# Performance work log

Hardware: AMD Instinct MI355X
Metric: run time of the kernel (lower is better)

The kernel has to match this reference:

```python
import jax, jax.numpy as jnp
import numpy as np
import math

D = 768
H = 8
DH = D // H
T = 4
MODES = 16
NUM_CLASSES = 14


def setup_inputs() -> dict:
    key = jax.random.key(0)
    ks = iter(jax.random.split(key, 64))
    B, S = 256, 512
    inp = {}
    inp['x_feat'] = jax.random.normal(next(ks), (B, S, D), dtype=jnp.float32)
    # attention pool
    inp['pool_w'] = jax.random.normal(next(ks), (D, 1), dtype=jnp.float32) * 0.02
    inp['pool_b'] = jnp.zeros((1,), dtype=jnp.float32)
    # per-block params, stacked over T
    def pstack(shape, scale=0.02):
        return jax.random.normal(next(ks), (T,) + shape, dtype=jnp.float32) * scale
    inp['w_q'] = pstack((D, D)); inp['w_k'] = pstack((D, D)); inp['w_v'] = pstack((D, D))
    inp['b_qkv'] = jnp.zeros((T, 3 * D), dtype=jnp.float32)
    inp['w_o'] = pstack((D, D)); inp['b_o'] = jnp.zeros((T, D), dtype=jnp.float32)
    inp['ln1_g'] = jnp.ones((T, D), dtype=jnp.float32); inp['ln1_b'] = jnp.zeros((T, D), dtype=jnp.float32)
    inp['ln2_g'] = jnp.ones((T, D), dtype=jnp.float32); inp['ln2_b'] = jnp.zeros((T, D), dtype=jnp.float32)
    inp['scale_real'] = pstack((MODES, D)); inp['scale_imag'] = pstack((MODES, D))
    inp['proj_w'] = pstack((D, D)); inp['proj_b'] = jnp.zeros((T, D), dtype=jnp.float32)
    inp['bn_g'] = jnp.ones((T, D), dtype=jnp.float32); inp['bn_b'] = jnp.zeros((T, D), dtype=jnp.float32)
    inp['gate'] = jnp.full((T,), 0.5, dtype=jnp.float32)
    inp['scale_attn'] = jnp.ones((T,), dtype=jnp.float32)
    inp['scale_denoise'] = jnp.ones((T,), dtype=jnp.float32)
    # fuse MLP + classifier
    inp['f1_w'] = jax.random.normal(next(ks), (D, 256), dtype=jnp.float32) * 0.02
    inp['f1_b'] = jnp.zeros((256,), dtype=jnp.float32)
    inp['f1_bn_g'] = jnp.ones((256,), dtype=jnp.float32); inp['f1_bn_b'] = jnp.zeros((256,), dtype=jnp.float32)
    inp['f2_w'] = jax.random.normal(next(ks), (256, 128), dtype=jnp.float32) * 0.02
    inp['f2_b'] = jnp.zeros((128,), dtype=jnp.float32)
    inp['f2_bn_g'] = jnp.ones((128,), dtype=jnp.float32); inp['f2_bn_b'] = jnp.zeros((128,), dtype=jnp.float32)
    inp['cls_w'] = jax.random.normal(next(ks), (128, NUM_CLASSES), dtype=jnp.float32) * 0.02
    inp['cls_b'] = jnp.zeros((NUM_CLASSES,), dtype=jnp.float32)
    return inp


def _layernorm(x, g, b, eps=1e-5):
    mu = jnp.mean(x, axis=-1, keepdims=True)
    var = jnp.var(x, axis=-1, keepdims=True)
    return (x - mu) * jax.lax.rsqrt(var + eps) * g + b


def _bn_eval(x, g, b, eps=1e-5):
    # eval-mode BatchNorm1d with running_mean=0, running_var=1
    return x * (g / jnp.sqrt(1.0 + eps)) + b


def _forward(x_feat, pool_w, pool_b, w_q, w_k, w_v, b_qkv, w_o, b_o,
             ln1_g, ln1_b, ln2_g, ln2_b, scale_real, scale_imag, proj_w, proj_b,
             bn_g, bn_b, gate, scale_attn, scale_denoise,
             f1_w, f1_b, f1_bn_g, f1_bn_b, f2_w, f2_b, f2_bn_g, f2_bn_b,
             cls_w, cls_b):
    B, S, _ = x_feat.shape
    # attention pool: softmax over seq of a scalar score per token
    scores = x_feat @ pool_w + pool_b          # [B,S,1]
    weights = jax.nn.softmax(scores, axis=1)
    z = jnp.sum(weights * x_feat, axis=1)      # [B,D]

    def classify(z):
        h = jax.nn.relu(_bn_eval(z @ f1_w + f1_b, f1_bn_g, f1_bn_b))
        h = jax.nn.relu(_bn_eval(h @ f2_w + f2_b, f2_bn_g, f2_bn_b))
        return h @ cls_w + cls_b

    logits_sum = jnp.zeros((B, NUM_CLASSES), dtype=x_feat.dtype)
    for t in range(T):
        bq, bk, bv = b_qkv[t, :D], b_qkv[t, D:2 * D], b_qkv[t, 2 * D:]
        # query: single token z [B,1,D]; keys/values: x_feat [B,S,D]
        q = (z @ w_q[t].T + bq).reshape(B, H, 1, DH)
        k = (x_feat @ w_k[t].T + bk).reshape(B, S, H, DH).transpose(0, 2, 1, 3)
        v = (x_feat @ w_v[t].T + bv).reshape(B, S, H, DH).transpose(0, 2, 1, 3)
        att = jax.nn.softmax(jnp.einsum('bhqd,bhsd->bhqs', q, k) / math.sqrt(DH), axis=-1)
        o = jnp.einsum('bhqs,bhsd->bhqd', att, v).reshape(B, D)
        z_attn = o @ w_o[t].T + b_o[t]
        z1 = _layernorm(z + scale_attn[t] * z_attn, ln1_g[t], ln1_b[t])
        # fft denoise: keep first MODES freq bins scaled by mean of complex filter per mode
        z_freq = jnp.fft.fft(z1, axis=1)                        # [B,D] complex
        filt = jnp.mean(scale_real[t] + 1j * scale_imag[t], axis=1)  # [MODES] complex
        keep = z_freq[:, :MODES] * filt[None, :]
        z_filtered = jnp.concatenate([keep, jnp.zeros((B, D - MODES), dtype=z_freq.dtype)], axis=1)
        z_spatial = jnp.fft.ifft(z_filtered, axis=1).real
        z_den = z_spatial @ proj_w[t].T + proj_b[t]
        z2 = _layernorm(z1 + scale_denoise[t] * z_den, ln2_g[t], ln2_b[t])
        g = jax.nn.sigmoid(gate[t])
        z3 = g * z2 + (1.0 - g) * z
        z = _bn_eval(z3, bn_g[t], bn_b[t])
        logits_sum = logits_sum + classify(z)
    return logits_sum / T


def reference(x_feat, pool_w, pool_b, w_q, w_k, w_v, b_qkv, w_o, b_o,
              ln1_g, ln1_b, ln2_g, ln2_b, scale_real, scale_imag, proj_w, proj_b,
              bn_g, bn_b, gate, scale_attn, scale_denoise,
              f1_w, f1_b, f1_bn_g, f1_bn_b, f2_w, f2_b, f2_bn_g, f2_bn_b,
              cls_w, cls_b):
    return _forward(x_feat, pool_w, pool_b, w_q, w_k, w_v, b_qkv, w_o, b_o,
                    ln1_g, ln1_b, ln2_g, ln2_b, scale_real, scale_imag, proj_w, proj_b,
                    bn_g, bn_b, gate, scale_attn, scale_denoise,
                    f1_w, f1_b, f1_bn_g, f1_bn_b, f2_w, f2_b, f2_bn_g, f2_bn_b,
                    cls_w, cls_b)
```

## Files before the change

### kernel.cpp

```cpp
#include <hip/hip_runtime.h>
#include <math.h>


#define DEV __device__ __forceinline__

typedef unsigned int   uint32;
typedef unsigned short ushort_t;
typedef __attribute__((ext_vector_type(8))) short bf16x8;
typedef __attribute__((ext_vector_type(4))) float f32x4;
typedef __attribute__((ext_vector_type(2))) float f32x2;

constexpr int Bv  = 256;
constexpr int Sv  = 512;
constexpr int Dv  = 768;
constexpr int Hv  = 8;
constexpr int DHv = 96;
constexpr int NCv = 14;

constexpr size_t ZL  = 196608;
constexpr size_t XWL = 1572864;
constexpr size_t WL  = 2359296;
constexpr size_t WT  = 589824;

DEV float4 ld4(const float* p) { return *reinterpret_cast<const float4*>(p); }

DEV ushort_t f2bf(float f) {
    uint32 u = __float_as_uint(f);
    u += 0x7FFFu + ((u >> 16) & 1u);
    return (ushort_t)(u >> 16);
}
DEV float bf2f(ushort_t h) { return __uint_as_float((uint32)h << 16); }
DEV void split2(float f, ushort_t& hi, ushort_t& lo) {
    hi = f2bf(f);
    lo = f2bf(f - bf2f(hi));
}
DEV uint2 pack4(float4 v) {
    return make_uint2((uint32)f2bf(v.x) | ((uint32)f2bf(v.y) << 16),
                      (uint32)f2bf(v.z) | ((uint32)f2bf(v.w) << 16));
}
DEV float bflo(uint32 u) { return __uint_as_float(u << 16); }
DEV float bfhi(uint32 u) { return __uint_as_float(u & 0xFFFF0000u); }

DEV f32x2 bfpair(uint32 u) {
    f32x2 r;
    r.x = __uint_as_float(u << 16);
    r.y = __uint_as_float(u & 0xFFFF0000u);
    return r;
}

DEV f32x2 pkfma(f32x2 a, f32x2 b, f32x2 c) {
    f32x2 d;
    asm("v_pk_fma_f32 %0, %1, %2, %3" : "=v"(d) : "v"(a), "v"(b), "v"(c));
    return d;
}

DEV void glds16(const void* g, void* l) {
    __builtin_amdgcn_global_load_lds(
        (const __attribute__((address_space(1))) void*)g,
        (__attribute__((address_space(3))) void*)l, 16, 0, 0);
}

__global__ __launch_bounds__(512, 4)
void pool_cvt_kernel(const float* __restrict__ x, const float* __restrict__ pool_w,
                     ushort_t* __restrict__ xbf,
                     float* __restrict__ pacc, float2* __restrict__ pml)
{
    __shared__ float qks[Dv];
    const int b = blockIdx.x, half = blockIdx.y;
    const int tid = threadIdx.x, wave = tid >> 6, lane = tid & 63;
    for (int i = tid; i < Dv / 4; i += 512)
        *reinterpret_cast<float4*>(&qks[i * 4]) = ld4(pool_w + i * 4);
    __syncthreads();

    const int row0 = half * 256 + wave * 32;
    const float* base = x + ((size_t)b * Sv + row0) * Dv + 4 * lane;

    float4 acc[3];
#pragma unroll
    for (int j = 0; j < 3; ++j) acc[j] = make_float4(0.f, 0.f, 0.f, 0.f);
    float m = -INFINITY, l = 0.f;

    float4 c0[3], c1[3];
#pragma unroll
    for (int j = 0; j < 3; ++j) { c0[j] = ld4(base + 256 * j); c1[j] = ld4(base + Dv + 256 * j); }

    for (int it = 0; it < 16; ++it) {
        float4 n0_[3], n1_[3];
        if (it < 15) {
            const float* nb = base + (size_t)(2 * it + 2) * Dv;
#pragma unroll
            for (int j = 0; j < 3; ++j) { n0_[j] = ld4(nb + 256 * j); n1_[j] = ld4(nb + Dv + 256 * j); }
        }
        ushort_t* ob = xbf + ((size_t)b * Sv + row0 + 2 * it) * Dv + 4 * lane;
#pragma unroll
        for (int j = 0; j < 3; ++j) *reinterpret_cast<uint2*>(ob + 256 * j) = pack4(c0[j]);
#pragma unroll
        for (int j = 0; j < 3; ++j) *reinterpret_cast<uint2*>(ob + Dv + 256 * j) = pack4(c1[j]);
        float p0 = 0.f, p1 = 0.f;
#pragma unroll
        for (int j = 0; j < 3; ++j) {
            const float4 q4 = *reinterpret_cast<const float4*>(&qks[4 * lane + 256 * j]);
            p0 = fmaf(q4.x, c0[j].x, p0); p0 = fmaf(q4.y, c0[j].y, p0);
            p0 = fmaf(q4.z, c0[j].z, p0); p0 = fmaf(q4.w, c0[j].w, p0);
            p1 = fmaf(q4.x, c1[j].x, p1); p1 = fmaf(q4.y, c1[j].y, p1);
            p1 = fmaf(q4.z, c1[j].z, p1); p1 = fmaf(q4.w, c1[j].w, p1);
        }
#pragma unroll
        for (int dd = 1; dd < 64; dd <<= 1) { p0 += __shfl_xor(p0, dd); p1 += __shfl_xor(p1, dd); }
        float mx = fmaxf(p0, p1);
        if (mx > m) {
            float r = __expf(m - mx); l *= r;
#pragma unroll
            for (int j = 0; j < 3; ++j) { acc[j].x *= r; acc[j].y *= r; acc[j].z *= r; acc[j].w *= r; }
            m = mx;
        }
        float w0 = __expf(p0 - m), w1 = __expf(p1 - m);
        l += w0 + w1;
#pragma unroll
        for (int j = 0; j < 3; ++j) {
            acc[j].x = fmaf(w1, c1[j].x, fmaf(w0, c0[j].x, acc[j].x));
            acc[j].y = fmaf(w1, c1[j].y, fmaf(w0, c0[j].y, acc[j].y));
            acc[j].z = fmaf(w1, c1[j].z, fmaf(w0, c0[j].z, acc[j].z));
            acc[j].w = fmaf(w1, c1[j].w, fmaf(w0, c0[j].w, acc[j].w));
        }
        if (it < 15) {
#pragma unroll
            for (int j = 0; j < 3; ++j) { c0[j] = n0_[j]; c1[j] = n1_[j]; }
        }
    }
    const int p = half * 8 + wave;
    const size_t pidx = (size_t)p * 256 + b;
#pragma unroll
    for (int j = 0; j < 3; ++j)
        *reinterpret_cast<float4*>(&pacc[pidx * Dv + 4 * lane + 256 * j]) = acc[j];
    if (lane == 0) pml[pidx] = make_float2(m, l);
}

__global__ __launch_bounds__(512, 4)
void attn_flash_kernel(const ushort_t* __restrict__ xbf, const float* __restrict__ Qk,
                       float* __restrict__ pacc, float2* __restrict__ pml, float scale)
{
    __shared__ ushort_t xs[2][16 * Dv];
    const int b = blockIdx.x, half = blockIdx.y;
    const int tid = threadIdx.x, wave = tid >> 6, lane = tid & 63;
    const int s0base = half * 256;

    const float* qp = Qk + ((size_t)b * Hv + wave) * Dv;
    f32x2 q2[6];
    {
        float4 a = ld4(qp + 8 * lane);
        float4 c = ld4(qp + 8 * lane + 4);
        float4 e = ld4(qp + 512 + 4 * lane);
        q2[0] = (f32x2){a.x, a.y}; q2[1] = (f32x2){a.z, a.w};
        q2[2] = (f32x2){c.x, c.y}; q2[3] = (f32x2){c.z, c.w};
        q2[4] = (f32x2){e.x, e.y}; q2[5] = (f32x2){e.z, e.w};
    }
    f32x2 acc2[6];
#pragma unroll
    for (int c = 0; c < 6; ++c) acc2[c] = (f32x2){0.f, 0.f};
    float m = -INFINITY, l = 0.f;

    auto stage = [&](int i, int buf) {
#pragma unroll
        for (int r = 0; r < 3; ++r) {
            int idx = wave * 3 + r;
            int off = idx * 1024 + lane * 16;
            int q   = off >> 9;
            int row = (q * 683) >> 11;
            int seg = q - row * 3;
            int colb = (seg << 9) + (off & 511);
            const char* src = (const char*)xbf +
                ((size_t)((size_t)b * Sv + s0base + i * 16 + row) * Dv) * 2 + colb;
            glds16(src, (char*)xs[buf] + idx * 1024);
        }
    };

    stage(0, 0);
    int cur = 0;
    for (int i = 0; i < 16; ++i) {
        __builtin_amdgcn_s_barrier();
        if (i < 15) {
            stage(i + 1, cur ^ 1);
            asm volatile("s_waitcnt vmcnt(3)" ::: "memory");
        } else {
            asm volatile("s_waitcnt vmcnt(0)" ::: "memory");
        }
        __builtin_amdgcn_s_barrier();
        __builtin_amdgcn_sched_barrier(0);

        const ushort_t* xt = xs[cur];
#pragma unroll
        for (int ch = 0; ch < 4; ++ch) {
            f32x2 xr[4][6];
            float s4[4];
#pragma unroll
            for (int j = 0; j < 4; ++j) {
                const ushort_t* rp = xt + (ch * 4 + j) * Dv;
                uint4 u0 = *reinterpret_cast<const uint4*>(rp + 8 * lane);
                uint2 u1 = *reinterpret_cast<const uint2*>(rp + 512 + 4 * lane);
                xr[j][0] = bfpair(u0.x); xr[j][1] = bfpair(u0.y);
                xr[j][2] = bfpair(u0.z); xr[j][3] = bfpair(u0.w);
                xr[j][4] = bfpair(u1.x); xr[j][5] = bfpair(u1.y);
                f32x2 s2 = (f32x2){0.f, 0.f};
#pragma unroll
                for (int c = 0; c < 6; ++c) s2 = pkfma(xr[j][c], q2[c], s2);
                s4[j] = s2.x + s2.y;
            }
            {
                const bool k0 = (lane & 1), k1 = (lane & 2);
                float sd0 = k0 ? s4[0] : s4[1];
                float rc0 = __shfl_xor(sd0, 1);
                float t0  = (k0 ? s4[1] : s4[0]) + rc0;
                float sd1 = k0 ? s4[2] : s4[3];
                float rc1 = __shfl_xor(sd1, 1);
                float t1  = (k0 ? s4[3] : s4[2]) + rc1;
                float sd2 = k1 ? t0 : t1;
                float rc2 = __shfl_xor(sd2, 2);
                float u   = (k1 ? t1 : t0) + rc2;
                u += __shfl_xor(u, 4);  u += __shfl_xor(u, 8);
                u += __shfl_xor(u, 16); u += __shfl_xor(u, 32);
                float b1 = __shfl_xor(u, 1);
                float b2 = __shfl_xor(u, 2);
                float b3 = __shfl_xor(u, 3);
                s4[0] = k1 ? (k0 ? b3 : b2) : (k0 ? b1 : u);
                s4[1] = k1 ? (k0 ? b2 : b3) : (k0 ? u  : b1);
                s4[2] = k1 ? (k0 ? b1 : u ) : (k0 ? b3 : b2);
                s4[3] = k1 ? (k0 ? u  : b1) : (k0 ? b2 : b3);
            }
#pragma unroll
            for (int j = 0; j < 4; ++j) s4[j] *= scale;
            float mx = fmaxf(fmaxf(s4[0], s4[1]), fmaxf(s4[2], s4[3]));
            if (mx > m) {
                float f = __expf(m - mx);
                l *= f;
#pragma unroll
                for (int c = 0; c < 6; ++c) { acc2[c].x *= f; acc2[c].y *= f; }
                m = mx;
            }
#pragma unroll
            for (int j = 0; j < 4; ++j) {
                float w = __expf(s4[j] - m);
                l += w;
                f32x2 w2 = (f32x2){w, w};
#pragma unroll
                for (int c = 0; c < 6; ++c) acc2[c] = pkfma(xr[j][c], w2, acc2[c]);
            }
        }
        cur ^= 1;
    }
    const size_t pidx = (size_t)(half * 256 + b) * Hv + wave;
    float* pb = pacc + pidx * Dv;
    *reinterpret_cast<float4*>(pb + 8 * lane)       = make_float4(acc2[0].x, acc2[0].y, acc2[1].x, acc2[1].y);
    *reinterpret_cast<float4*>(pb + 8 * lane + 4)   = make_float4(acc2[2].x, acc2[2].y, acc2[3].x, acc2[3].y);
    *reinterpret_cast<float4*>(pb + 512 + 4 * lane) = make_float4(acc2[4].x, acc2[4].y, acc2[5].x, acc2[5].y);
    if (lane == 0) pml[pidx] = make_float2(m, l);
}

template<int NH, int NP, bool WF32>
__global__ __launch_bounds__(256)
void merge_kernel(const float* __restrict__ pacc, const float2* __restrict__ pml,
                  ushort_t* __restrict__ obf, size_t loOff, float* __restrict__ of32)
{
    __shared__ float eS[NH * NP];
    const int b = blockIdx.x, tid = threadIdx.x;
    if (tid < NH) {
        float2 mls[NP];
        float mm = -INFINITY;
#pragma unroll
        for (int p = 0; p < NP; ++p) {
            mls[p] = pml[((size_t)p * 256 + b) * NH + tid];
            mm = fmaxf(mm, mls[p].x);
        }
        float ee[NP]; float L = 0.f;
#pragma unroll
        for (int p = 0; p < NP; ++p) { ee[p] = __expf(mls[p].x - mm); L += mls[p].y * ee[p]; }
        float inv = 1.f / L;
#pragma unroll
        for (int p = 0; p < NP; ++p) eS[tid * NP + p] = ee[p] * inv;
    }
    __syncthreads();
#pragma unroll
    for (int seg = 0; seg < NH * 3; ++seg) {
        int h = seg / 3;
        int d = (seg - h * 3) * 256 + tid;
        float v = 0.f;
#pragma unroll
        for (int p = 0; p < NP; ++p)
            v += pacc[((size_t)((size_t)p * 256 + b) * NH + h) * Dv + d] * eS[h * NP + p];
        size_t oi = ((size_t)b * NH + h) * Dv + d;
        ushort_t hi, lo; split2(v, hi, lo);
        obf[oi] = hi; obf[oi + loOff] = lo;
        if (WF32) of32[oi] = v;
    }
}

template<int MODE, bool OBF>
__global__ __launch_bounds__(256)
void mgemm_kernel(const ushort_t* __restrict__ A, size_t aLo,
                  const ushort_t* __restrict__ W, size_t wLo,
                  const float* __restrict__ bias, void* __restrict__ outp,
                  size_t oLo)
{
    constexpr int BN = (MODE == 2) ? 96 : 64;
    constexpr int BK = (MODE == 1) ? 32 : 64;
    constexpr int NJ = BN / 32;
    constexpr int KTOT = (MODE == 1) ? 96 : 768;
    constexpr int NSTEP = KTOT / BK;
    constexpr int CH = BK / 8;
    constexpr int CA = (64 * BK) / 512;
    constexpr int CB = (BN * BK) / 512;
    constexpr int NC = 2 * (CA + CB) / 4;
    constexpr int LDA = (MODE == 2) ? 6144 : 768;
    constexpr int LDW = (MODE == 1) ? 96 : 768;
    constexpr int LDO = (MODE == 1) ? 6144 : 768;
    constexpr int WCW = (MODE == 2) ? 48 : 32;
    constexpr int RSH = (BK == 64) ? 7 : 6;

    __shared__ ushort_t As[2][2][64 * BK];
    __shared__ ushort_t Bs[2][2][BN * BK];

    const int tid = threadIdx.x, wave = tid >> 6, lane = tid & 63;
    const int n0 = blockIdx.x * BN;
    const int m0 = blockIdx.y * 64;
    const int h  = (MODE == 1) ? blockIdx.z : ((MODE == 2) ? blockIdx.x : 0);
    const int acol = (MODE == 1) ? h * 96 : ((MODE == 2) ? h * 768 : 0);
    const ushort_t* Wb = W + ((MODE == 1) ? (size_t)h * 768 * 96 : (size_t)0);
    const int ocol = (MODE == 1) ? h * 768 : 0;

    const int wr = wave >> 1, wc = wave & 1;
    const int l15 = lane & 15, kg = lane >> 4;

    auto stage = [&](int kt, int buf) {
#pragma unroll
        for (int hl = 0; hl < 2; ++hl) {
            const ushort_t* Ap = A + (hl ? aLo : 0);
            const ushort_t* Wp = Wb + (hl ? wLo : 0);
#pragma unroll
            for (int c = 0; c < CA / 4; ++c) {
                int call = wave + 4 * c;
                int off = call * 1024 + lane * 16;
                int row = off >> RSH;
                int chunk = (off & (2 * BK - 1)) >> 4;
                int sw = chunk ^ (row & (CH - 1));
                const ushort_t* src = Ap + (size_t)(m0 + row) * LDA + acol + kt + sw * 8;
                glds16(src, (char*)As[buf][hl] + call * 1024);
            }
#pragma unroll
            for (int c = 0; c < CB / 4; ++c) {
                int call = wave + 4 * c;
                int off = call * 1024 + lane * 16;
                int row = off >> RSH;
                int chunk = (off & (2 * BK - 1)) >> 4;
                int sw = chunk ^ (row & (CH - 1));
                const ushort_t* src = Wp + (size_t)(n0 + row) * LDW + kt + sw * 8;
                glds16(src, (char*)Bs[buf][hl] + call * 1024);
            }
        }
    };

    f32x4 acc[2][NJ];
#pragma unroll
    for (int i = 0; i < 2; ++i)
#pragma unroll
        for (int j = 0; j < NJ; ++j) acc[i][j] = (f32x4){0.f, 0.f, 0.f, 0.f};

    stage(0, 0);
    int cur = 0;
    for (int s = 0; s < NSTEP; ++s) {
        __builtin_amdgcn_s_barrier();
        if (s + 1 < NSTEP) {
            stage((s + 1) * BK, cur ^ 1);
            asm volatile("s_waitcnt vmcnt(%0)" :: "i"(NC) : "memory");
        } else {
            asm volatile("s_waitcnt vmcnt(0)" ::: "memory");
        }
        __builtin_amdgcn_s_barrier();
        __builtin_amdgcn_sched_barrier(0);

        const ushort_t* ah_ = As[cur][0];
        const ushort_t* al_ = As[cur][1];
        const ushort_t* bh_ = Bs[cur][0];
        const ushort_t* bl_ = Bs[cur][1];
#pragma unroll
        for (int kw = 0; kw < BK / 32; ++kw) {
            const int kb = kw * 4;
            bf16x8 ah[2], al[2], bh[NJ], bl[NJ];
#pragma unroll
            for (int i = 0; i < 2; ++i) {
                int r = wr * 32 + i * 16 + l15;
                int c = (kb + kg) ^ (r & (CH - 1));
                ah[i] = *reinterpret_cast<const bf16x8*>(&ah_[r * BK + c * 8]);
                al[i] = *reinterpret_cast<const bf16x8*>(&al_[r * BK + c * 8]);
            }
#pragma unroll
            for (int j = 0; j < NJ; ++j) {
                int r = wc * WCW + j * 16 + l15;
                int c = (kb + kg) ^ (r & (CH - 1));
                bh[j] = *reinterpret_cast<const bf16x8*>(&bh_[r * BK + c * 8]);
                bl[j] = *reinterpret_cast<const bf16x8*>(&bl_[r * BK + c * 8]);
            }
#pragma unroll
            for (int i = 0; i < 2; ++i)
#pragma unroll
                for (int j = 0; j < NJ; ++j) {
                    acc[i][j] = __builtin_amdgcn_mfma_f32_16x16x32_bf16(al[i], bh[j], acc[i][j], 0, 0, 0);
                    acc[i][j] = __builtin_amdgcn_mfma_f32_16x16x32_bf16(ah[i], bl[j], acc[i][j], 0, 0, 0);
                    acc[i][j] = __builtin_amdgcn_mfma_f32_16x16x32_bf16(ah[i], bh[j], acc[i][j], 0, 0, 0);
                }
        }
        cur ^= 1;
    }

#pragma unroll
    for (int i = 0; i < 2; ++i)
#pragma unroll
        for (int j = 0; j < NJ; ++j) {
            int rg = m0 + wr * 32 + i * 16 + kg * 4;
            int cg = n0 + wc * WCW + j * 16 + l15;
            float bv = bias ? bias[cg] : 0.f;
#pragma unroll
            for (int reg = 0; reg < 4; ++reg) {
                float v = acc[i][j][reg] + bv;
                size_t oi = (size_t)(rg + reg) * LDO + ocol + cg;
                if (OBF) {
                    ushort_t hi, lo; split2(v, hi, lo);
                    ((ushort_t*)outp)[oi] = hi;
                    ((ushort_t*)outp)[oi + oLo] = lo;
                } else {
                    ((float*)outp)[oi] = v;
                }
            }
        }
}

__global__ __launch_bounds__(256)
void cvt3_kernel(const float* __restrict__ wq, const float* __restrict__ wv,
                 const float* __restrict__ wo, ushort_t* __restrict__ dst)
{
    const int bid = blockIdx.x;
    const int w = bid / 1152;
    const int off = (bid - w * 1152) * 2048 + threadIdx.x * 8;
    const float* src = (w == 0) ? wq : (w == 1) ? wv : wo;
    ushort_t hi[8], lo[8];
#pragma unroll
    for (int e = 0; e < 8; ++e) split2(src[off + e], hi[e], lo[e]);
    ushort_t* base = dst + (size_t)w * (2 * WL);
    *reinterpret_cast<uint4*>(base + off) = *reinterpret_cast<uint4*>(hi);
    *reinterpret_cast<uint4*>(base + WL + off) = *reinterpret_cast<uint4*>(lo);
}

__global__ __launch_bounds__(256)
void wkT_kernel(const float* __restrict__ w_k, ushort_t* __restrict__ wkT)
{
    __shared__ float tile[96][65];
    const int n0 = blockIdx.x * 64;
    const int th = blockIdx.y;
    const int t = th >> 3, h = th & 7;
    const float* src = w_k + ((size_t)t * Dv + h * DHv) * Dv + n0;
    for (int idx = threadIdx.x; idx < 96 * 64; idx += 256) {
        int j = idx >> 6, n = idx & 63;
        tile[j][n] = src[(size_t)j * Dv + n];
    }
    __syncthreads();
    for (int idx = threadIdx.x; idx < 64 * 96; idx += 256) {
        int n = idx / 96, j = idx - n * 96;
        ushort_t hi, lo; split2(tile[j][n], hi, lo);
        size_t oi = ((size_t)th * Dv + n0 + n) * DHv + j;
        wkT[oi] = hi; wkT[oi + WL] = lo;
    }
}

__global__ __launch_bounds__(256)
void pre1_kernel(float* __restrict__ twc, float* __restrict__ tws,
                 const float* __restrict__ sr, const float* __restrict__ si,
                 float* __restrict__ filt)
{
    __shared__ float red[8];
    const int bid = blockIdx.x;
    if (bid < 48) {
        int idx = bid * 256 + threadIdx.x;
        int k = idx / Dv, n = idx % Dv;
        int r = (k * n) % Dv;
        float ang = (float)r * (float)(6.283185307179586 / 768.0);
        twc[idx] = cosf(ang);
        tws[idx] = sinf(ang);
    } else {
        int tk = bid - 48;
        const float* a  = sr + (size_t)tk * Dv;
        const float* b2 = si + (size_t)tk * Dv;
        float s1 = 0.f, s2 = 0.f;
#pragma unroll
        for (int j = 0; j < 3; ++j) {
            int c = threadIdx.x + 256 * j;
            s1 += a[c]; s2 += b2[c];
        }
        int wave = threadIdx.x >> 6, lane = threadIdx.x & 63;
#pragma unroll
        for (int dd = 1; dd < 64; dd <<= 1) { s1 += __shfl_xor(s1, dd); s2 += __shfl_xor(s2, dd); }
        if (lane == 0) { red[wave * 2] = s1; red[wave * 2 + 1] = s2; }
        __syncthreads();
        if (threadIdx.x == 0) {
            filt[tk * 2]     = (red[0] + red[2] + red[4] + red[6]) * (1.f / 768.f);
            filt[tk * 2 + 1] = (red[1] + red[3] + red[5] + red[7]) * (1.f / 768.f);
        }
    }
}

__global__ __launch_bounds__(256)
void cs_kernel(const float* __restrict__ proj_w, const float* __restrict__ twc,
               const float* __restrict__ tws, float* __restrict__ csC,
               float* __restrict__ csS)
{
    const int i = blockIdx.x * 256 + threadIdx.x;
    const int k = blockIdx.y;
    const int t = blockIdx.z;
    const float* pr = proj_w + ((size_t)t * Dv + i) * Dv;
    const float* tc = twc + (size_t)k * Dv;
    const float* ts = tws + (size_t)k * Dv;
    float ac = 0.f, as = 0.f;
    for (int n = 0; n < Dv; ++n) {
        float p = pr[n];
        ac = fmaf(p, tc[n], ac);
        as = fmaf(p, ts[n], as);
    }
    csC[((size_t)t * 16 + k) * Dv + i] = ac * (1.f / 768.f);
    csS[((size_t)t * 16 + k) * Dv + i] = as * (1.f / 768.f);
}

__global__ __launch_bounds__(256)
void lnden_kernel(float* __restrict__ z, ushort_t* __restrict__ zbf,
                  const float* __restrict__ za,
                  const float* __restrict__ g1, const float* __restrict__ b1,
                  const float* __restrict__ g2, const float* __restrict__ b2,
                  const float* __restrict__ bng, const float* __restrict__ bnb,
                  const float* __restrict__ gate_p, const float* __restrict__ sa_p,
                  const float* __restrict__ sd_p,
                  const float* __restrict__ twc, const float* __restrict__ tws,
                  const float* __restrict__ filt_t,
                  const float* __restrict__ csC_t, const float* __restrict__ csS_t,
                  const float* __restrict__ pb_t,
                  const float* __restrict__ f1w, const float* __restrict__ f1b,
                  const float* __restrict__ f1g, const float* __restrict__ f1bb,
                  const float* __restrict__ f2w, const float* __restrict__ f2b,
                  const float* __restrict__ f2g, const float* __restrict__ f2bb,
                  const float* __restrict__ clw, const float* __restrict__ clb,
                  float* __restrict__ outp, int t)
{
    const int b = blockIdx.x, tid = threadIdx.x;
    const int wave = tid >> 6, lane = tid & 63;
    __shared__ float red[8];
    __shared__ float dred[4][32];
    __shared__ float fin[32];
    __shared__ float kr[16], ki[16];
    __shared__ float zs[768];
    __shared__ float h1s[256];
    __shared__ float h2s[128];

    const float sa = sa_p[0];
    float v[3], zo[3];
    float s = 0.f, s2 = 0.f;
#pragma unroll
    for (int j = 0; j < 3; ++j) {
        int c = tid + 256 * j;
        zo[j] = z[(size_t)b * Dv + c];
        float val = zo[j] + sa * za[(size_t)b * Dv + c];
        v[j] = val; s += val; s2 += val * val;
    }
#pragma unroll
    for (int dd = 1; dd < 64; dd <<= 1) { s += __shfl_xor(s, dd); s2 += __shfl_xor(s2, dd); }
    if (lane == 0) { red[wave * 2] = s; red[wave * 2 + 1] = s2; }
    __syncthreads();
    {
        const float mean = (red[0] + red[2] + red[4] + red[6]) * (1.f / 768.f);
        const float var  = (red[1] + red[3] + red[5] + red[7]) * (1.f / 768.f) - mean * mean;
        const float rstd = rsqrtf(var + 1e-5f);
#pragma unroll
        for (int j = 0; j < 3; ++j) {
            int c = tid + 256 * j;
            v[j] = (v[j] - mean) * rstd * g1[c] + b1[c];
        }
    }
    float Fc[16], Fs[16];
#pragma unroll
    for (int k = 0; k < 16; ++k) { Fc[k] = 0.f; Fs[k] = 0.f; }
#pragma unroll
    for (int j = 0; j < 3; ++j) {
        int c = tid + 256 * j;
#pragma unroll
        for (int k = 0; k < 16; ++k) {
            Fc[k] = fmaf(v[j], twc[k * Dv + c], Fc[k]);
            Fs[k] = fmaf(v[j], tws[k * Dv + c], Fs[k]);
        }
    }
#pragma unroll
    for (int dd = 1; dd < 64; dd <<= 1) {
#pragma unroll
        for (int k = 0; k < 16; ++k) { Fc[k] += __shfl_xor(Fc[k], dd); Fs[k] += __shfl_xor(Fs[k], dd); }
    }
    if (lane == 0) {
#pragma unroll
        for (int k = 0; k < 16; ++k) { dred[wave][k] = Fc[k]; dred[wave][16 + k] = Fs[k]; }
    }
    __syncthreads();
    if (tid < 32) fin[tid] = dred[0][tid] + dred[1][tid] + dred[2][tid] + dred[3][tid];
    __syncthreads();
    if (tid < 16) {
        float Sc = fin[tid], Ss = fin[16 + tid];
        float fr = filt_t[tid * 2], fi = filt_t[tid * 2 + 1];
        kr[tid] = Sc * fr + Ss * fi;
        ki[tid] = Sc * fi - Ss * fr;
    }
    __syncthreads();

    const float sd  = sd_p[0];
    const float gv  = 1.f / (1.f + expf(-gate_p[0]));
    const float bnc = 1.f / sqrtf(1.f + 1e-5f);
    float w3[3];
    s = 0.f; s2 = 0.f;
#pragma unroll
    for (int j = 0; j < 3; ++j) {
        int c = tid + 256 * j;
        float den = pb_t[c];
#pragma unroll
        for (int k = 0; k < 16; ++k) {
            den = fmaf(kr[k], csC_t[k * Dv + c], den);
            den = fmaf(-ki[k], csS_t[k * Dv + c], den);
        }
        float val = v[j] + sd * den;
        w3[j] = val; s += val; s2 += val * val;
    }
#pragma unroll
    for (int dd = 1; dd < 64; dd <<= 1) { s += __shfl_xor(s, dd); s2 += __shfl_xor(s2, dd); }
    if (lane == 0) { red[wave * 2] = s; red[wave * 2 + 1] = s2; }
    __syncthreads();
    const float mean2 = (red[0] + red[2] + red[4] + red[6]) * (1.f / 768.f);
    const float var2  = (red[1] + red[3] + red[5] + red[7]) * (1.f / 768.f) - mean2 * mean2;
    const float rstd2 = rsqrtf(var2 + 1e-5f);
#pragma unroll
    for (int j = 0; j < 3; ++j) {
        int c = tid + 256 * j;
        float z2v = (w3[j] - mean2) * rstd2 * g2[c] + b2[c];
        float z3v = gv * z2v + (1.f - gv) * zo[j];
        float zn  = z3v * (bng[c] * bnc) + bnb[c];
        z[(size_t)b * Dv + c] = zn;
        ushort_t hi, lo; split2(zn, hi, lo);
        zbf[(size_t)b * Dv + c] = hi;
        zbf[(size_t)b * Dv + c + ZL] = lo;
        zs[c] = zn;
    }
    __syncthreads();
    float h = f1b[tid];
    for (int d = 0; d < 768; ++d) h = fmaf(zs[d], f1w[(size_t)d * 256 + tid], h);
    h = h * (f1g[tid] * bnc) + f1bb[tid];
    h1s[tid] = fmaxf(h, 0.f);
    __syncthreads();
    if (tid < 128) {
        float h2 = f2b[tid];
        for (int i2 = 0; i2 < 256; ++i2) h2 = fmaf(h1s[i2], f2w[(size_t)i2 * 128 + tid], h2);
        h2 = h2 * (f2g[tid] * bnc) + f2bb[tid];
        h2s[tid] = fmaxf(h2, 0.f);
    }
    __syncthreads();
    if (tid < NCv) {
        float lg = clb[tid];
        for (int i2 = 0; i2 < 128; ++i2) lg = fmaf(h2s[i2], clw[(size_t)i2 * NCv + tid], lg);
        lg *= 0.25f;
        if (t == 0) outp[(size_t)b * NCv + tid] = lg;
        else        outp[(size_t)b * NCv + tid] += lg;
    }
}

extern "C" void kernel_launch(void* const* d_in, const int* in_sizes, int n_in,
                              void* d_out, int out_size, void* d_ws, size_t ws_size,
                              hipStream_t stream)
{
    (void)in_sizes; (void)n_in; (void)out_size; (void)ws_size;
    const float* x      = (const float*)d_in[0];
    const float* pool_w = (const float*)d_in[1];
    const float* w_q   = (const float*)d_in[3];
    const float* w_k   = (const float*)d_in[4];
    const float* w_v   = (const float*)d_in[5];
    const float* b_qkv = (const float*)d_in[6];
    const float* w_o   = (const float*)d_in[7];
    const float* b_o   = (const float*)d_in[8];
    const float* ln1_g = (const float*)d_in[9];
    const float* ln1_b = (const float*)d_in[10];
    const float* ln2_g = (const float*)d_in[11];
    const float* ln2_b = (const float*)d_in[12];
    const float* s_re  = (const float*)d_in[13];
    const float* s_im  = (const float*)d_in[14];
    const float* proj_w= (const float*)d_in[15];
    const float* proj_b= (const float*)d_in[16];
    const float* bn_g  = (const float*)d_in[17];
    const float* bn_b  = (const float*)d_in[18];
    const float* gate  = (const float*)d_in[19];
    const float* s_at  = (const float*)d_in[20];
    const float* s_dn  = (const float*)d_in[21];
    const float* f1w   = (const float*)d_in[22];
    const float* f1b   = (const float*)d_in[23];
    const float* f1g   = (const float*)d_in[24];
    const float* f1bb  = (const float*)d_in[25];
    const float* f2w   = (const float*)d_in[26];
    const float* f2b   = (const float*)d_in[27];
    const float* f2g   = (const float*)d_in[28];
    const float* f2bb  = (const float*)d_in[29];
    const float* clw   = (const float*)d_in[30];
    const float* clb   = (const float*)d_in[31];
    float* out = (float*)d_out;

    float* ws   = (float*)d_ws;
    float* twc  = ws;
    float* tws  = twc + 12288;
    float* filt = tws + 12288;
    float* csC  = filt + 128;
    float* csS  = csC + 49152;
    float* z    = csS + 49152;
    float* za   = z + 196608;
    float* Qk   = za + 196608;
    float* pacc = Qk + 1572864;
    float* pmlf = pacc + 3145728;
    ushort_t* xbf  = (ushort_t*)(pmlf + 8192);
    ushort_t* zbf  = xbf + 100663296;
    ushort_t* qbf  = zbf + 2 * ZL;
    ushort_t* xwbf = qbf + 2 * ZL;
    ushort_t* obf  = xwbf + 2 * XWL;
    ushort_t* wspl = obf + 2 * ZL;
    ushort_t* wkT  = wspl + 6 * WL;
    float2* pml = (float2*)pmlf;
    ushort_t* wqbf = wspl;
    ushort_t* wvbf = wspl + 2 * WL;
    ushort_t* wobf = wspl + 4 * WL;

    pre1_kernel<<<112, 256, 0, stream>>>(twc, tws, s_re, s_im, filt);
    cs_kernel<<<dim3(3, 16, 4), 256, 0, stream>>>(proj_w, twc, tws, csC, csS);
    cvt3_kernel<<<3456, 256, 0, stream>>>(w_q, w_v, w_o, wspl);
    wkT_kernel<<<dim3(12, 32), 256, 0, stream>>>(w_k, wkT);

    pool_cvt_kernel<<<dim3(256, 2), 512, 0, stream>>>(x, pool_w, xbf, pacc, pml);
    merge_kernel<1, 16, true><<<256, 256, 0, stream>>>(pacc, pml, zbf, ZL, z);

    const float iscale = (float)(1.0 / sqrt(96.0));
    for (int t = 0; t < 4; ++t) {
        mgemm_kernel<0, true><<<dim3(12, 4), 256, 0, stream>>>(
            zbf, ZL, wqbf + (size_t)t * WT, WL, b_qkv + (size_t)t * 2304, qbf, ZL);
        mgemm_kernel<1, false><<<dim3(12, 4, 8), 256, 0, stream>>>(
            qbf, ZL, wkT + (size_t)t * WT, WL, nullptr, Qk, 0);
        attn_flash_kernel<<<dim3(256, 2), 512, 0, stream>>>(xbf, Qk, pacc, pml, iscale);
        merge_kernel<8, 2, false><<<256, 256, 0, stream>>>(pacc, pml, xwbf, XWL, nullptr);
        mgemm_kernel<2, true><<<dim3(8, 4), 256, 0, stream>>>(
            xwbf, XWL, wvbf + (size_t)t * WT, WL, b_qkv + (size_t)t * 2304 + 1536, obf, ZL);
        mgemm_kernel<0, false><<<dim3(12, 4), 256, 0, stream>>>(
            obf, ZL, wobf + (size_t)t * WT, WL, b_o + (size_t)t * Dv, za, 0);
        lnden_kernel<<<256, 256, 0, stream>>>(
            z, zbf, za,
            ln1_g + (size_t)t * Dv, ln1_b + (size_t)t * Dv,
            ln2_g + (size_t)t * Dv, ln2_b + (size_t)t * Dv,
            bn_g + (size_t)t * Dv, bn_b + (size_t)t * Dv,
            gate + t, s_at + t, s_dn + t,
            twc, tws, filt + (size_t)t * 32,
            csC + (size_t)t * 12288, csS + (size_t)t * 12288,
            proj_b + (size_t)t * Dv,
            f1w, f1b, f1g, f1bb, f2w, f2b, f2g, f2bb,
            clw, clb, out, t);
    }
}
```

Baseline: 975.6 us.

## Restructure attention: two heads per wave, direct global loads, four row slices

The flash attention kernel drops its LDS double-buffered staging. Each wave now handles two heads over a 128-row slice and reads bf16 rows straight from global memory with register prefetch, so every loaded x row serves two heads instead of one. The sequence is split into four partial slices per batch instead of two, so the partial-accumulator workspace doubles and the merge kernel combines four partials. This removes the LDS traffic and barriers, at the cost of per-wave redundant global reads (four waves read the same rows) and more merge work.

```diff
diff --git a/kernel.cpp b/kernel.cpp
--- a/kernel.cpp
+++ b/kernel.cpp
@@ -38,8 +38,6 @@
     return make_uint2((uint32)f2bf(v.x) | ((uint32)f2bf(v.y) << 16),
                       (uint32)f2bf(v.z) | ((uint32)f2bf(v.w) << 16));
 }
-DEV float bflo(uint32 u) { return __uint_as_float(u << 16); }
-DEV float bfhi(uint32 u) { return __uint_as_float(u & 0xFFFF0000u); }
 
 DEV f32x2 bfpair(uint32 u) {
     f32x2 r;
@@ -140,120 +138,140 @@
 void attn_flash_kernel(const ushort_t* __restrict__ xbf, const float* __restrict__ Qk,
                        float* __restrict__ pacc, float2* __restrict__ pml, float scale)
 {
-    __shared__ ushort_t xs[2][16 * Dv];
     const int b = blockIdx.x, half = blockIdx.y;
     const int tid = threadIdx.x, wave = tid >> 6, lane = tid & 63;
-    const int s0base = half * 256;
-
-    const float* qp = Qk + ((size_t)b * Hv + wave) * Dv;
-    f32x2 q2[6];
+    const int hg = wave & 3, slice = wave >> 2;
+    const int h0 = 2 * hg, h1 = h0 + 1;
+    const int row0 = half * 256 + slice * 128;
+
+    f32x2 q0[6], q1[6];
     {
-        float4 a = ld4(qp + 8 * lane);
-        float4 c = ld4(qp + 8 * lane + 4);
-        float4 e = ld4(qp + 512 + 4 * lane);
-        q2[0] = (f32x2){a.x, a.y}; q2[1] = (f32x2){a.z, a.w};
-        q2[2] = (f32x2){c.x, c.y}; q2[3] = (f32x2){c.z, c.w};
-        q2[4] = (f32x2){e.x, e.y}; q2[5] = (f32x2){e.z, e.w};
-    }
-    f32x2 acc2[6];
-#pragma unroll
-    for (int c = 0; c < 6; ++c) acc2[c] = (f32x2){0.f, 0.f};
-    float m = -INFINITY, l = 0.f;
-
-    auto stage = [&](int i, int buf) {
-#pragma unroll
-        for (int r = 0; r < 3; ++r) {
-            int idx = wave * 3 + r;
-            int off = idx * 1024 + lane * 16;
-            int q   = off >> 9;
-            int row = (q * 683) >> 11;
-            int seg = q - row * 3;
-            int colb = (seg << 9) + (off & 511);
-            const char* src = (const char*)xbf +
-                ((size_t)((size_t)b * Sv + s0base + i * 16 + row) * Dv) * 2 + colb;
-            glds16(src, (char*)xs[buf] + idx * 1024);
-        }
-    };
-
-    stage(0, 0);
-    int cur = 0;
-    for (int i = 0; i < 16; ++i) {
-        __builtin_amdgcn_s_barrier();
-        if (i < 15) {
-            stage(i + 1, cur ^ 1);
-            asm volatile("s_waitcnt vmcnt(3)" ::: "memory");
-        } else {
-            asm volatile("s_waitcnt vmcnt(0)" ::: "memory");
-        }
-        __builtin_amdgcn_s_barrier();
-        __builtin_amdgcn_sched_barrier(0);
-
-        const ushort_t* xt = xs[cur];
-#pragma unroll
-        for (int ch = 0; ch < 4; ++ch) {
-            f32x2 xr[4][6];
-            float s4[4];
-#pragma unroll
-            for (int j = 0; j < 4; ++j) {
-                const ushort_t* rp = xt + (ch * 4 + j) * Dv;
-                uint4 u0 = *reinterpret_cast<const uint4*>(rp + 8 * lane);
-                uint2 u1 = *reinterpret_cast<const uint2*>(rp + 512 + 4 * lane);
-                xr[j][0] = bfpair(u0.x); xr[j][1] = bfpair(u0.y);
-                xr[j][2] = bfpair(u0.z); xr[j][3] = bfpair(u0.w);
-                xr[j][4] = bfpair(u1.x); xr[j][5] = bfpair(u1.y);
-                f32x2 s2 = (f32x2){0.f, 0.f};
-#pragma unroll
-                for (int c = 0; c < 6; ++c) s2 = pkfma(xr[j][c], q2[c], s2);
-                s4[j] = s2.x + s2.y;
+        const float* qp0 = Qk + ((size_t)b * Hv + h0) * Dv + 4 * lane;
+        const float* qp1 = Qk + ((size_t)b * Hv + h1) * Dv + 4 * lane;
+#pragma unroll
+        for (int s = 0; s < 3; ++s) {
+            float4 a = ld4(qp0 + s * 256);
+            float4 c = ld4(qp1 + s * 256);
+            q0[2 * s]     = (f32x2){a.x, a.y}; q0[2 * s + 1] = (f32x2){a.z, a.w};
+            q1[2 * s]     = (f32x2){c.x, c.y}; q1[2 * s + 1] = (f32x2){c.z, c.w};
+        }
+    }
+    f32x2 a0[6], a1[6];
+#pragma unroll
+    for (int c = 0; c < 6; ++c) { a0[c] = (f32x2){0.f, 0.f}; a1[c] = (f32x2){0.f, 0.f}; }
+    float m0 = -INFINITY, l0 = 0.f, m1 = -INFINITY, l1 = 0.f;
+
+    const ushort_t* base = xbf + ((size_t)b * Sv + row0) * Dv + 4 * lane;
+
+    uint2 c0[3], c1[3];
+#pragma unroll
+    for (int s = 0; s < 3; ++s) {
+        c0[s] = *reinterpret_cast<const uint2*>(base + s * 256);
+        c1[s] = *reinterpret_cast<const uint2*>(base + Dv + s * 256);
+    }
+
+    for (int it = 0; it < 64; ++it) {
+        uint2 n0[3], n1[3];
+        if (it < 63) {
+            const ushort_t* nb = base + (size_t)(2 * it + 2) * Dv;
+#pragma unroll
+            for (int s = 0; s < 3; ++s) {
+                n0[s] = *reinterpret_cast<const uint2*>(nb + s * 256);
+                n1[s] = *reinterpret_cast<const uint2*>(nb + Dv + s * 256);
             }
-            {
-                const bool k0 = (lane & 1), k1 = (lane & 2);
-                float sd0 = k0 ? s4[0] : s4[1];
-                float rc0 = __shfl_xor(sd0, 1);
-                float t0  = (k0 ? s4[1] : s4[0]) + rc0;
-                float sd1 = k0 ? s4[2] : s4[3];
-                float rc1 = __shfl_xor(sd1, 1);
-                float t1  = (k0 ? s4[3] : s4[2]) + rc1;
-                float sd2 = k1 ? t0 : t1;
-                float rc2 = __shfl_xor(sd2, 2);
-                float u   = (k1 ? t1 : t0) + rc2;
-                u += __shfl_xor(u, 4);  u += __shfl_xor(u, 8);
-                u += __shfl_xor(u, 16); u += __shfl_xor(u, 32);
-                float b1 = __shfl_xor(u, 1);
-                float b2 = __shfl_xor(u, 2);
-                float b3 = __shfl_xor(u, 3);
-                s4[0] = k1 ? (k0 ? b3 : b2) : (k0 ? b1 : u);
-                s4[1] = k1 ? (k0 ? b2 : b3) : (k0 ? u  : b1);
-                s4[2] = k1 ? (k0 ? b1 : u ) : (k0 ? b3 : b2);
-                s4[3] = k1 ? (k0 ? u  : b1) : (k0 ? b2 : b3);
+        }
+        f32x2 xf0[6], xf1[6];
+#pragma unroll
+        for (int s = 0; s < 3; ++s) {
+            xf0[2 * s] = bfpair(c0[s].x); xf0[2 * s + 1] = bfpair(c0[s].y);
+            xf1[2 * s] = bfpair(c1[s].x); xf1[2 * s + 1] = bfpair(c1[s].y);
+        }
+        f32x2 t00 = (f32x2){0.f, 0.f}, t01 = t00, t10 = t00, t11 = t00;
+#pragma unroll
+        for (int c = 0; c < 6; ++c) {
+            t00 = pkfma(xf0[c], q0[c], t00);
+            t01 = pkfma(xf0[c], q1[c], t01);
+            t10 = pkfma(xf1[c], q0[c], t10);
+            t11 = pkfma(xf1[c], q1[c], t11);
+        }
+        float s4[4];
+        s4[0] = t00.x + t00.y;
+        s4[1] = t01.x + t01.y;
+        s4[2] = t10.x + t10.y;
+        s4[3] = t11.x + t11.y;
+        {
+            const bool k0 = (lane & 1), k1 = (lane & 2);
+            float sd0 = k0 ? s4[0] : s4[1];
+            float rc0 = __shfl_xor(sd0, 1);
+            float t0  = (k0 ? s4[1] : s4[0]) + rc0;
+            float sd1 = k0 ? s4[2] : s4[3];
+            float rc1 = __shfl_xor(sd1, 1);
+            float t1  = (k0 ? s4[3] : s4[2]) + rc1;
+            float sd2 = k1 ? t0 : t1;
+            float rc2 = __shfl_xor(sd2, 2);
+            float u   = (k1 ? t1 : t0) + rc2;
+            u += __shfl_xor(u, 4);  u += __shfl_xor(u, 8);
+            u += __shfl_xor(u, 16); u += __shfl_xor(u, 32);
+            float b1 = __shfl_xor(u, 1);
+            float b2 = __shfl_xor(u, 2);
+            float b3 = __shfl_xor(u, 3);
+            s4[0] = k1 ? (k0 ? b3 : b2) : (k0 ? b1 : u);
+            s4[1] = k1 ? (k0 ? b2 : b3) : (k0 ? u  : b1);
+            s4[2] = k1 ? (k0 ? b1 : u ) : (k0 ? b3 : b2);
+            s4[3] = k1 ? (k0 ? u  : b1) : (k0 ? b2 : b3);
+        }
+#pragma unroll
+        for (int j = 0; j < 4; ++j) s4[j] *= scale;
+        {
+            float mx = fmaxf(s4[0], s4[2]);
+            if (mx > m0) {
+                float f = __expf(m0 - mx); l0 *= f;
+#pragma unroll
+                for (int c = 0; c < 6; ++c) { a0[c].x *= f; a0[c].y *= f; }
+                m0 = mx;
             }
-#pragma unroll
-            for (int j = 0; j < 4; ++j) s4[j] *= scale;
-            float mx = fmaxf(fmaxf(s4[0], s4[1]), fmaxf(s4[2], s4[3]));
-            if (mx > m) {
-                float f = __expf(m - mx);
-                l *= f;
-#pragma unroll
-                for (int c = 0; c < 6; ++c) { acc2[c].x *= f; acc2[c].y *= f; }
-                m = mx;
+            float w0 = __expf(s4[0] - m0), w1 = __expf(s4[2] - m0);
+            l0 += w0 + w1;
+            f32x2 w02 = (f32x2){w0, w0}, w12 = (f32x2){w1, w1};
+#pragma unroll
+            for (int c = 0; c < 6; ++c) a0[c] = pkfma(xf1[c], w12, pkfma(xf0[c], w02, a0[c]));
+        }
+        {
+            float mx = fmaxf(s4[1], s4[3]);
+            if (mx > m1) {
+                float f = __expf(m1 - mx); l1 *= f;
+#pragma unroll
+                for (int c = 0; c < 6; ++c) { a1[c].x *= f; a1[c].y *= f; }
+                m1 = mx;
             }
-#pragma unroll
-            for (int j = 0; j < 4; ++j) {
-                float w = __expf(s4[j] - m);
-                l += w;
-                f32x2 w2 = (f32x2){w, w};
-#pragma unroll
-                for (int c = 0; c < 6; ++c) acc2[c] = pkfma(xr[j][c], w2, acc2[c]);
-            }
-        }
-        cur ^= 1;
-    }
-    const size_t pidx = (size_t)(half * 256 + b) * Hv + wave;
-    float* pb = pacc + pidx * Dv;
-    *reinterpret_cast<float4*>(pb + 8 * lane)       = make_float4(acc2[0].x, acc2[0].y, acc2[1].x, acc2[1].y);
-    *reinterpret_cast<float4*>(pb + 8 * lane + 4)   = make_float4(acc2[2].x, acc2[2].y, acc2[3].x, acc2[3].y);
-    *reinterpret_cast<float4*>(pb + 512 + 4 * lane) = make_float4(acc2[4].x, acc2[4].y, acc2[5].x, acc2[5].y);
-    if (lane == 0) pml[pidx] = make_float2(m, l);
+            float w0 = __expf(s4[1] - m1), w1 = __expf(s4[3] - m1);
+            l1 += w0 + w1;
+            f32x2 w02 = (f32x2){w0, w0}, w12 = (f32x2){w1, w1};
+#pragma unroll
+            for (int c = 0; c < 6; ++c) a1[c] = pkfma(xf1[c], w12, pkfma(xf0[c], w02, a1[c]));
+        }
+        if (it < 63) {
+#pragma unroll
+            for (int s = 0; s < 3; ++s) { c0[s] = n0[s]; c1[s] = n1[s]; }
+        }
+    }
+
+    const int p = half * 2 + slice;
+    const size_t pidx0 = ((size_t)p * 256 + b) * Hv + h0;
+    const size_t pidx1 = pidx0 + 1;
+    float* pb0 = pacc + pidx0 * Dv + 4 * lane;
+    float* pb1 = pacc + pidx1 * Dv + 4 * lane;
+#pragma unroll
+    for (int s = 0; s < 3; ++s) {
+        *reinterpret_cast<float4*>(pb0 + s * 256) =
+            make_float4(a0[2 * s].x, a0[2 * s].y, a0[2 * s + 1].x, a0[2 * s + 1].y);
+        *reinterpret_cast<float4*>(pb1 + s * 256) =
+            make_float4(a1[2 * s].x, a1[2 * s].y, a1[2 * s + 1].x, a1[2 * s + 1].y);
+    }
+    if (lane == 0) {
+        pml[pidx0] = make_float2(m0, l0);
+        pml[pidx1] = make_float2(m1, l1);
+    }
 }
 
 template<int NH, int NP, bool WF32>
@@ -718,8 +736,8 @@
     float* za   = z + 196608;
     float* Qk   = za + 196608;
     float* pacc = Qk + 1572864;
-    float* pmlf = pacc + 3145728;
-    ushort_t* xbf  = (ushort_t*)(pmlf + 8192);
+    float* pmlf = pacc + 6291456;
+    ushort_t* xbf  = (ushort_t*)(pmlf + 16384);
     ushort_t* zbf  = xbf + 100663296;
     ushort_t* qbf  = zbf + 2 * ZL;
     ushort_t* xwbf = qbf + 2 * ZL;
@@ -746,7 +764,7 @@
         mgemm_kernel<1, false><<<dim3(12, 4, 8), 256, 0, stream>>>(
             qbf, ZL, wkT + (size_t)t * WT, WL, nullptr, Qk, 0);
         attn_flash_kernel<<<dim3(256, 2), 512, 0, stream>>>(xbf, Qk, pacc, pml, iscale);
-        merge_kernel<8, 2, false><<<256, 256, 0, stream>>>(pacc, pml, xwbf, XWL, nullptr);
+        merge_kernel<8, 4, false><<<256, 256, 0, stream>>>(pacc, pml, xwbf, XWL, nullptr);
         mgemm_kernel<2, true><<<dim3(8, 4), 256, 0, stream>>>(
             xwbf, XWL, wvbf + (size_t)t * WT, WL, b_qkv + (size_t)t * 2304 + 1536, obf, ZL);
         mgemm_kernel<0, false><<<dim3(12, 4), 256, 0, stream>>>(
```

Measured after the change: 948.8 us. 1.03x faster.
